# Performance work log

Measured on AMD Instinct MI355X. Metric: run time of the kernel, lower is better.

## Reference

```python
import jax, jax.numpy as jnp
import numpy as np

C = 64
CR = C // 8  # reduced channels for Q/K


def _conv1x1(x, W, b):
    # 1x1 conv == per-pixel linear over channels: x [b,c,h,w], W [o,c], b [o]
    return jnp.einsum('bchw,oc->bohw', x, W) + b[None, :, None, None]


def setup_inputs() -> dict:
    key = jax.random.key(0)
    ks = jax.random.split(key, 12)
    b, c, h, w = 8, C, 48, 48
    s = 1.0 / np.sqrt(c)
    inp = {
        'x1': jax.random.normal(ks[0], (b, c, h, w), jnp.float32),
        'x2': jax.random.normal(ks[1], (b, c, h, w), jnp.float32),
        'Wqk1': jax.random.normal(ks[2], (2 * CR, c), jnp.float32) * s,
        'bqk1': jnp.zeros((2 * CR,), jnp.float32),
        'Wqk2': jax.random.normal(ks[3], (2 * CR, c), jnp.float32) * s,
        'bqk2': jnp.zeros((2 * CR,), jnp.float32),
        'Wv1': jax.random.normal(ks[4], (c, c), jnp.float32) * s,
        'bv1': jnp.zeros((c,), jnp.float32),
        'Wv2': jax.random.normal(ks[5], (c, c), jnp.float32) * s,
        'bv2': jnp.zeros((c,), jnp.float32),
        'gamma': jnp.zeros((1,), jnp.float32) + 0.1,  # nonzero so output depends on attn
        'beta': jnp.zeros((1,), jnp.float32) + 0.1,
    }
    return inp


def reference(x1, x2, Wqk1, bqk1, Wqk2, bqk2, Wv1, bv1, Wv2, bv2, gamma, beta):
    b, c, h, w = x1.shape
    n = h * w
    qk1 = _conv1x1(x1, Wqk1, bqk1)
    qk2 = _conv1x1(x2, Wqk2, bqk2)
    q1, k1 = qk1[:, :CR], qk1[:, CR:]
    q2, k2 = qk2[:, :CR], qk2[:, CR:]
    # flatten spatial: [b, cr, n]
    q1 = q1.reshape(b, CR, n); k1 = k1.reshape(b, CR, n)
    q2 = q2.reshape(b, CR, n); k2 = k2.reshape(b, CR, n)
    v1 = _conv1x1(x1, Wv1, bv1).reshape(b, c, n)
    v2 = _conv1x1(x2, Wv2, bv2).reshape(b, c, n)
    # attn[b,i,j] = softmax_j( q[:, :, i] . k[:, :, j] )
    attn1 = jax.nn.softmax(jnp.einsum('bci,bcj->bij', q1, k1), axis=-1)
    attn2 = jax.nn.softmax(jnp.einsum('bci,bcj->bij', q2, k2), axis=-1)
    # out[:, :, j] = sum_i v[:, :, i] * attn[:, i, j]
    o1 = jnp.einsum('bci,bij->bcj', v1, attn2).reshape(b, c, h, w) * gamma + x1
    o2 = jnp.einsum('bci,bij->bcj', v2, attn1).reshape(b, c, h, w) * beta + x2
    return (o1, o2)
```

## Files before the change

kernel.cpp:

```cpp
#include <hip/hip_runtime.h>
#include <hip/hip_bf16.h>

#define NB   8
#define CCH  64
#define CR8  8
#define NPX  2304
#define BCN  (NB*CCH*NPX)
#define LOG2E 1.4426950408889634f

typedef short  short8   __attribute__((ext_vector_type(8)));
typedef unsigned short ushort8t __attribute__((ext_vector_type(8)));
typedef float  float4t  __attribute__((ext_vector_type(4)));
typedef float  float16t __attribute__((ext_vector_type(16)));

static __device__ __forceinline__ float fexp2(float x) {
    return __builtin_amdgcn_exp2f(x);
}
static __device__ __forceinline__ unsigned short bf16r(float f) {
    return (unsigned short)((__float_as_uint(f) + 0x8000u) >> 16);
}
static __device__ __forceinline__ unsigned int pack_bf16(float lo, float hi) {
    const unsigned int ul = __float_as_uint(lo) + 0x8000u;
    const unsigned int uh = __float_as_uint(hi) + 0x8000u;
    return __builtin_amdgcn_perm(uh, ul, 0x07060302u);
}
static __device__ __forceinline__ short8 pack8(const float* f) {
    union { unsigned int u[4]; short8 s; } r;
    #pragma unroll
    for (int j = 0; j < 4; j++) r.u[j] = pack_bf16(f[2*j], f[2*j+1]);
    return r.s;
}

static __device__ __forceinline__ void build_bfrag(const float16t sc, short8* bf) {
    unsigned int d[4][2];
    #pragma unroll
    for (int q = 0; q < 4; q++) {
        #pragma unroll
        for (int m = 0; m < 2; m++)
            d[q][m] = pack_bf16(fexp2(sc[4*q + 2*m]), fexp2(sc[4*q + 2*m + 1]));
    }
    #pragma unroll
    for (int kp = 0; kp < 2; kp++) {
        union { unsigned int u[4]; short8 s; } r;
        #pragma unroll
        for (int m = 0; m < 2; m++) {
            unsigned int x = d[2*kp][m];
            unsigned int y = d[2*kp + 1][m];
            asm("v_permlane32_swap_b32 %0, %1" : "+v"(x), "+v"(y));
            r.u[m]     = x;
            r.u[2 + m] = y;
        }
        bf[kp] = r.s;
    }
}

#define WS_QB1 0
#define WS_KB1 (WS_QB1 + 147456)
#define WS_QB2 (WS_KB1 + 147456)
#define WS_KB2 (WS_QB2 + 147456)
#define WS_V1  (WS_KB2 + 147456)
#define WS_V2  (WS_V1 + BCN/2)
#define WS_PD  (WS_V2 + BCN/2)

__global__ __launch_bounds__(256) void proj_kernel(
    const float* __restrict__ x1, const float* __restrict__ x2,
    const float* __restrict__ Wqk1, const float* __restrict__ bqk1,
    const float* __restrict__ Wqk2, const float* __restrict__ bqk2,
    const float* __restrict__ Wv1,  const float* __restrict__ bv1,
    const float* __restrict__ Wv2,  const float* __restrict__ bv2,
    float* __restrict__ ws, float* __restrict__ out)
{
    const int t    = threadIdx.x;
    const int lane = t & 63;
    const int w    = t >> 6;
    const int n16  = lane & 15;
    const int c4   = lane >> 4;
    const int nt   = w & 1;
    const int mh   = w >> 1;
    const int b    = blockIdx.y;
    const int px   = blockIdx.x * 32 + nt * 16 + n16;

    const float* xsb[2];
    xsb[0] = x1 + ((size_t)b * CCH) * NPX + px;
    xsb[1] = x2 + ((size_t)b * CCH) * NPX + px;

    float xr[2][16];
    short8 bfrag[2][2];
    #pragma unroll
    for (int st = 0; st < 2; st++) {
        #pragma unroll
        for (int ch = 0; ch < 2; ch++) {
            #pragma unroll
            for (int j = 0; j < 8; j++)
                xr[st][ch * 8 + j] = xsb[st][(ch * 32 + c4 * 8 + j) * NPX];
            bfrag[st][ch] = pack8(&xr[st][ch * 8]);
        }
    }

    if (mh == 0) {
        #pragma unroll
        for (int st = 0; st < 2; st++) {
            float* outs = out + (st ? (size_t)BCN : 0);
            #pragma unroll
            for (int e = 0; e < 16; e++) {
                const int ch = (e >> 3) * 32 + c4 * 8 + (e & 7);
                outs[((size_t)b * CCH + ch) * NPX + px] = xr[st][e];
            }
        }
    }

    float4t acc[5];
    #pragma unroll
    for (int mt = 0; mt < 5; mt++) { acc[mt][0]=0.f; acc[mt][1]=0.f; acc[mt][2]=0.f; acc[mt][3]=0.f; }

    #pragma unroll
    for (int mt = 0; mt < 5; mt++) {
        const int mi  = mh * 5 + mt;
        const int isqk = (mi < 2);
        const int st  = isqk ? (mi & 1) : (mi >= 6);
        const float* Wb;
        int rowbase;
        if (isqk) { Wb = (mi == 0) ? Wqk1 : Wqk2; rowbase = 0; }
        else      { Wb = (mi >= 6) ? Wv2 : Wv1; rowbase = (mi - (mi >= 6 ? 6 : 2)) * 16; }
        const float* wrow = Wb + (size_t)(rowbase + n16) * 64 + c4 * 8;

        const short8 bf0 = st ? bfrag[1][0] : bfrag[0][0];
        const short8 bf1 = st ? bfrag[1][1] : bfrag[0][1];

        #pragma unroll
        for (int ch = 0; ch < 2; ch++) {
            float fa[8];
            const float4 a0 = *(const float4*)(wrow + ch * 32);
            const float4 a1 = *(const float4*)(wrow + ch * 32 + 4);
            fa[0] = a0.x; fa[1] = a0.y; fa[2] = a0.z; fa[3] = a0.w;
            fa[4] = a1.x; fa[5] = a1.y; fa[6] = a1.z; fa[7] = a1.w;
            acc[mt] = __builtin_amdgcn_mfma_f32_16x16x32_bf16(
                pack8(fa), ch ? bf1 : bf0, acc[mt], 0, 0, 0);
        }
    }

    #pragma unroll
    for (int mt = 0; mt < 5; mt++) {
        const int mi = mh * 5 + mt;
        if (mi < 2) {
            const int st = mi & 1;
            const float* bqk = st ? bqk2 : bqk1;
            unsigned short* qb = (unsigned short*)(ws + (st ? WS_QB2 : WS_QB1));
            unsigned short* kb = (unsigned short*)(ws + (st ? WS_KB2 : WS_KB1));
            const size_t rbase = (size_t)(b * NPX + px) * 16;
            #pragma unroll
            for (int r = 0; r < 4; r++) {
                const int oc = c4 * 4 + r;
                const float val = acc[mt][r] + bqk[oc];
                if (oc < 8)
                    qb[rbase + oc] = bf16r(val * LOG2E);
                else
                    kb[rbase + (oc - 8)] = bf16r(val);
            }
            ushort8t zq, zk;
            #pragma unroll
            for (int e = 0; e < 8; e++) { zq[e] = 0; zk[e] = 0; }
            zk[0] = 0x3F80; zk[1] = 0x3F80;
            if (c4 == 0) *(ushort8t*)(qb + rbase + 8) = zq;
            if (c4 == 2) *(ushort8t*)(kb + rbase + 8) = zk;
        } else {
            const int st = (mi >= 6);
            const int vt_ = mi - (st ? 6 : 2);
            const float* bv = st ? bv2 : bv1;
            unsigned short* v = (unsigned short*)(ws + (st ? WS_V2 : WS_V1));
            #pragma unroll
            for (int r = 0; r < 4; r++) {
                const int oc = vt_ * 16 + c4 * 4 + r;
                const float val = acc[mt][r] + bv[oc];
                v[((size_t)b * CCH + oc) * NPX + px] = bf16r(val);
            }
        }
    }
}

__global__ __launch_bounds__(256) void stats_kernel(float* __restrict__ ws)
{
    const int t  = threadIdx.x;
    const int w  = t >> 6;
    const int n  = t & 31;
    const int h  = (t & 63) >> 5;
    const int jsb = blockIdx.x;
    const int iq  = blockIdx.y;
    const int ab  = blockIdx.z;
    const int b   = ab & 7;
    const int a   = ab >> 3;

    const unsigned short* qb = (const unsigned short*)(ws + (a ? WS_QB2 : WS_QB1));
    const unsigned short* kb = (const unsigned short*)(ws + (a ? WS_KB2 : WS_KB1));
    float* pd = ws + WS_PD;

    __shared__ float red[4][288];

    const int j = jsb * 128 + w * 32 + n;
    const short8 kfrag = *(const short8*)(kb + (size_t)(b * NPX + j) * 16 + h * 8);

    const unsigned short* qp = qb + (size_t)(b * NPX + iq * 288 + n) * 16 + h * 8;
    short8 qf = *(const short8*)qp;

    for (int ib = 0; ib < 9; ib++) {
        qp += 512;
        short8 qn = qf;
        if (ib + 1 < 9) qn = *(const short8*)qp;
        float16t acc = {};
        acc = __builtin_amdgcn_mfma_f32_32x32x16_bf16(kfrag, qf, acc, 0, 0, 0);
        float s0 = 0.f, s1 = 0.f, s2 = 0.f, s3 = 0.f;
        #pragma unroll
        for (int r = 0; r < 4; r++) {
            s0 += fexp2(acc[4 * r + 0]);
            s1 += fexp2(acc[4 * r + 1]);
            s2 += fexp2(acc[4 * r + 2]);
            s3 += fexp2(acc[4 * r + 3]);
        }
        float ssum = (s0 + s1) + (s2 + s3);
        ssum += __shfl_xor(ssum, 32);
        if (h == 0) red[w][ib * 32 + n] = ssum;
        qf = qn;
    }
    __syncthreads();
    for (int idx = t; idx < 288; idx += 256)
        pd[((size_t)ab * 18 + jsb) * NPX + iq * 288 + idx] =
            red[0][idx] + red[1][idx] + red[2][idx] + red[3][idx];
}

__global__ __launch_bounds__(256) void merge_fold(float* __restrict__ ws)
{
    const float* pd = ws + WS_PD;
    const int t  = threadIdx.x;
    const int il = t & 63;
    const int pg = t >> 6;
    const int i  = blockIdx.x * 64 + il;
    const int ab = blockIdx.y;
    const int b  = ab & 7;
    const int a  = ab >> 3;

    __shared__ float red[4][64];

    const float* pb = pd + (size_t)ab * 18 * NPX + i;
    float d = 0.f;
    #pragma unroll
    for (int c = pg; c < 18; c += 4)
        d += pb[(size_t)c * NPX];
    red[pg][il] = d;
    __syncthreads();

    if (t < 64) {
        const float dt = (red[0][t] + red[1][t]) + (red[2][t] + red[3][t]);
        const float m = -__log2f(dt);
        const unsigned short mh = bf16r(m);
        __hip_bfloat16 hb; *(unsigned short*)&hb = mh;
        const unsigned short ml = bf16r(m - __bfloat162float(hb));
        unsigned short* qb = (unsigned short*)(ws + (a ? WS_QB2 : WS_QB1));
        const size_t rbase = (size_t)(b * NPX + blockIdx.x * 64 + t) * 16;
        qb[rbase + 8] = mh;
        qb[rbase + 9] = ml;
    }
}

__global__ __launch_bounds__(256) void out_kernel(
    const float* __restrict__ gamma, const float* __restrict__ beta,
    const float* __restrict__ ws, float* __restrict__ out)
{
    const int t  = threadIdx.x;
    const int jt = blockIdx.x;
    const int b  = blockIdx.y;
    const int z  = blockIdx.z;
    const int o  = z >> 2;
    const int ihalf = z & 3;

    const int a = o ? 0 : 1;
    const unsigned short* qb = (const unsigned short*)(ws + (a ? WS_QB2 : WS_QB1));
    const unsigned short* kb = (const unsigned short*)(ws + (a ? WS_KB2 : WS_KB1));
    const unsigned short* v  = (const unsigned short*)(ws + (o ? WS_V2 : WS_V1));
    const float  scale = o ? beta[0] : gamma[0];

    __shared__ unsigned short vt[2][64][72];

    const int lane = t & 63;
    const int w    = t >> 6;
    const int n    = lane & 31;
    const int h    = lane >> 5;
    const int jh   = w & 1;
    const int ih   = w >> 1;

    const int j0 = jt * 64 + jh * 32;

    const short8 kfrag = *(const short8*)(kb + (size_t)(b * NPX + j0 + n) * 16 + h * 8);

    const int c0 = t >> 3, s80 = (t & 7) * 8;
    const int c1 = (t + 256) >> 3, s81 = ((t + 256) & 7) * 8;

    const int ibase = ihalf * 576;
    const unsigned short* vp0 = v + ((size_t)b * CCH + c0) * NPX + ibase + s80;
    const unsigned short* vp1 = v + ((size_t)b * CCH + c1) * NPX + ibase + s81;
    const unsigned short* qp  = qb + (size_t)(b * NPX + ibase + ih * 32 + n) * 16 + h * 8;

    {
        const float4 va = *(const float4*)vp0;
        const float4 vb = *(const float4*)vp1;
        *(float4*)&vt[0][c0][s80] = va;
        *(float4*)&vt[0][c1][s81] = vb;
    }
    short8 qf = *(const short8*)qp;

    float16t oacc0 = {}, oacc1 = {};
    int cur = 0;

    for (int it = 0; it < 9; it++) {
        vp0 += 64; vp1 += 64; qp += 64 * 16;
        float4 vn0, vn1;
        short8 qn = qf;
        if (it + 1 < 9) {
            vn0 = *(const float4*)vp0;
            vn1 = *(const float4*)vp1;
            qn  = *(const short8*)qp;
        }

        __syncthreads();

        float16t sc = {};
        sc = __builtin_amdgcn_mfma_f32_32x32x16_bf16(qf, kfrag, sc, 0, 0, 0);

        short8 bf[2];
        build_bfrag(sc, bf);

        {
            const short8 a0 = *(const short8*)&vt[cur][n][ih * 32 + 0 * 16 + h * 8];
            const short8 a1 = *(const short8*)&vt[cur][32 + n][ih * 32 + 0 * 16 + h * 8];
            oacc0 = __builtin_amdgcn_mfma_f32_32x32x16_bf16(a0, bf[0], oacc0, 0, 0, 0);
            oacc1 = __builtin_amdgcn_mfma_f32_32x32x16_bf16(a1, bf[0], oacc1, 0, 0, 0);
            const short8 a2 = *(const short8*)&vt[cur][n][ih * 32 + 1 * 16 + h * 8];
            const short8 a3 = *(const short8*)&vt[cur][32 + n][ih * 32 + 1 * 16 + h * 8];
            oacc0 = __builtin_amdgcn_mfma_f32_32x32x16_bf16(a2, bf[1], oacc0, 0, 0, 0);
            oacc1 = __builtin_amdgcn_mfma_f32_32x32x16_bf16(a3, bf[1], oacc1, 0, 0, 0);
        }

        if (it + 1 < 9) {
            *(float4*)&vt[cur ^ 1][c0][s80] = vn0;
            *(float4*)&vt[cur ^ 1][c1][s81] = vn1;
        }

        qf = qn;
        cur ^= 1;
    }

    __syncthreads();
    float* comb = (float*)&vt[0][0][0];
    float* cb = comb + (size_t)jh * 2304 + (size_t)lane * 36;
    if (ih == 1) {
        *(float4*)(cb +  0) = *((const float4*)&oacc0 + 0);
        *(float4*)(cb +  4) = *((const float4*)&oacc0 + 1);
        *(float4*)(cb +  8) = *((const float4*)&oacc0 + 2);
        *(float4*)(cb + 12) = *((const float4*)&oacc0 + 3);
        *(float4*)(cb + 16) = *((const float4*)&oacc1 + 0);
        *(float4*)(cb + 20) = *((const float4*)&oacc1 + 1);
        *(float4*)(cb + 24) = *((const float4*)&oacc1 + 2);
        *(float4*)(cb + 28) = *((const float4*)&oacc1 + 3);
    }
    __syncthreads();
    if (ih == 0) {
        #pragma unroll
        for (int q = 0; q < 4; q++) {
            const float4 p0 = *(const float4*)(cb + q * 4);
            const float4 p1 = *(const float4*)(cb + 16 + q * 4);
            oacc0[4*q+0] += p0.x; oacc0[4*q+1] += p0.y; oacc0[4*q+2] += p0.z; oacc0[4*q+3] += p0.w;
            oacc1[4*q+0] += p1.x; oacc1[4*q+1] += p1.y; oacc1[4*q+2] += p1.z; oacc1[4*q+3] += p1.w;
        }
        float* outp = out + (o ? BCN : 0) + (b * CCH) * NPX + j0 + n;
        #pragma unroll
        for (int r = 0; r < 16; r++) {
            const int row = (r & 3) + 8 * (r >> 2) + 4 * h;
            atomicAdd(outp + row * NPX, oacc0[r] * scale);
            atomicAdd(outp + (32 + row) * NPX, oacc1[r] * scale);
        }
    }
}

extern "C" void kernel_launch(void* const* d_in, const int* in_sizes, int n_in,
                              void* d_out, int out_size, void* d_ws, size_t ws_size,
                              hipStream_t stream)
{
    const float* x1   = (const float*)d_in[0];
    const float* x2   = (const float*)d_in[1];
    const float* Wqk1 = (const float*)d_in[2];
    const float* bqk1 = (const float*)d_in[3];
    const float* Wqk2 = (const float*)d_in[4];
    const float* bqk2 = (const float*)d_in[5];
    const float* Wv1  = (const float*)d_in[6];
    const float* bv1  = (const float*)d_in[7];
    const float* Wv2  = (const float*)d_in[8];
    const float* bv2  = (const float*)d_in[9];
    const float* gamma = (const float*)d_in[10];
    const float* beta  = (const float*)d_in[11];
    float* out = (float*)d_out;
    float* ws  = (float*)d_ws;

    proj_kernel<<<dim3(72, 8), 256, 0, stream>>>(
        x1, x2, Wqk1, bqk1, Wqk2, bqk2, Wv1, bv1, Wv2, bv2, ws, out);
    stats_kernel<<<dim3(18, 8, 16), 256, 0, stream>>>(ws);
    merge_fold<<<dim3(36, 16), 256, 0, stream>>>(ws);
    out_kernel<<<dim3(36, 8, 8), 256, 0, stream>>>(gamma, beta, ws, out);
}
```

Measured before the change: 148.1 us.

## Fuse stats, merge and output kernels into persistent kernel with grid barriers

Replaces three separate launches (row-sum stats, merge/fold of softmax denominators, output attention-V product) with one persistent kernel of 1024 blocks that loops over work items and separates phases with atomic-counter global barriers. Barrier counters are reset by the projection kernel. The aim is to remove launch gaps and kernel-boundary drains between short phases. In exchange it needs all 1024 blocks co-resident (launch bounds 256,4 with 256 CUs) or the barrier deadlocks, and each barrier adds spin-wait cost.

```diff
diff --git a/kernel.cpp b/kernel.cpp
--- a/kernel.cpp
+++ b/kernel.cpp
@@ -61,6 +61,21 @@
 #define WS_V1  (WS_KB2 + 147456)
 #define WS_V2  (WS_V1 + BCN/2)
 #define WS_PD  (WS_V2 + BCN/2)
+#define WS_BAR (WS_PD + 16*18*NPX)
+
+#define FUSED_GRID 1024
+
+static __device__ __forceinline__ void gbar(unsigned int* bar, unsigned int target) {
+    __syncthreads();
+    if (threadIdx.x == 0) {
+        __threadfence();
+        __hip_atomic_fetch_add(bar, 1u, __ATOMIC_RELEASE, __HIP_MEMORY_SCOPE_AGENT);
+        while (__hip_atomic_load(bar, __ATOMIC_ACQUIRE, __HIP_MEMORY_SCOPE_AGENT) < target)
+            __builtin_amdgcn_s_sleep(2);
+        __threadfence();
+    }
+    __syncthreads();
+}
 
 __global__ __launch_bounds__(256) void proj_kernel(
     const float* __restrict__ x1, const float* __restrict__ x2,
@@ -80,6 +95,11 @@
     const int b    = blockIdx.y;
     const int px   = blockIdx.x * 32 + nt * 16 + n16;
 
+    if (blockIdx.x == 0 && blockIdx.y == 0 && t == 0) {
+        unsigned int* bar = (unsigned int*)(ws + WS_BAR);
+        bar[0] = 0; bar[1] = 0;
+    }
+
     const float* xsb[2];
     xsb[0] = x1 + ((size_t)b * CCH) * NPX + px;
     xsb[1] = x2 + ((size_t)b * CCH) * NPX + px;
@@ -178,204 +198,223 @@
     }
 }
 
-__global__ __launch_bounds__(256) void stats_kernel(float* __restrict__ ws)
+__global__ __launch_bounds__(256, 4) void fused_smo(
+    const float* __restrict__ gamma, const float* __restrict__ beta,
+    float* __restrict__ ws, float* __restrict__ out)
 {
-    const int t  = threadIdx.x;
-    const int w  = t >> 6;
-    const int n  = t & 31;
-    const int h  = (t & 63) >> 5;
-    const int jsb = blockIdx.x;
-    const int iq  = blockIdx.y;
-    const int ab  = blockIdx.z;
-    const int b   = ab & 7;
-    const int a   = ab >> 3;
-
-    const unsigned short* qb = (const unsigned short*)(ws + (a ? WS_QB2 : WS_QB1));
-    const unsigned short* kb = (const unsigned short*)(ws + (a ? WS_KB2 : WS_KB1));
-    float* pd = ws + WS_PD;
-
-    __shared__ float red[4][288];
-
-    const int j = jsb * 128 + w * 32 + n;
-    const short8 kfrag = *(const short8*)(kb + (size_t)(b * NPX + j) * 16 + h * 8);
-
-    const unsigned short* qp = qb + (size_t)(b * NPX + iq * 288 + n) * 16 + h * 8;
-    short8 qf = *(const short8*)qp;
-
-    for (int ib = 0; ib < 9; ib++) {
-        qp += 512;
-        short8 qn = qf;
-        if (ib + 1 < 9) qn = *(const short8*)qp;
-        float16t acc = {};
-        acc = __builtin_amdgcn_mfma_f32_32x32x16_bf16(kfrag, qf, acc, 0, 0, 0);
-        float s0 = 0.f, s1 = 0.f, s2 = 0.f, s3 = 0.f;
-        #pragma unroll
-        for (int r = 0; r < 4; r++) {
-            s0 += fexp2(acc[4 * r + 0]);
-            s1 += fexp2(acc[4 * r + 1]);
-            s2 += fexp2(acc[4 * r + 2]);
-            s3 += fexp2(acc[4 * r + 3]);
-        }
-        float ssum = (s0 + s1) + (s2 + s3);
-        ssum += __shfl_xor(ssum, 32);
-        if (h == 0) red[w][ib * 32 + n] = ssum;
-        qf = qn;
-    }
-    __syncthreads();
-    for (int idx = t; idx < 288; idx += 256)
-        pd[((size_t)ab * 18 + jsb) * NPX + iq * 288 + idx] =
-            red[0][idx] + red[1][idx] + red[2][idx] + red[3][idx];
-}
-
-__global__ __launch_bounds__(256) void merge_fold(float* __restrict__ ws)
-{
-    const float* pd = ws + WS_PD;
-    const int t  = threadIdx.x;
-    const int il = t & 63;
-    const int pg = t >> 6;
-    const int i  = blockIdx.x * 64 + il;
-    const int ab = blockIdx.y;
-    const int b  = ab & 7;
-    const int a  = ab >> 3;
-
-    __shared__ float red[4][64];
-
-    const float* pb = pd + (size_t)ab * 18 * NPX + i;
-    float d = 0.f;
-    #pragma unroll
-    for (int c = pg; c < 18; c += 4)
-        d += pb[(size_t)c * NPX];
-    red[pg][il] = d;
-    __syncthreads();
-
-    if (t < 64) {
-        const float dt = (red[0][t] + red[1][t]) + (red[2][t] + red[3][t]);
-        const float m = -__log2f(dt);
-        const unsigned short mh = bf16r(m);
-        __hip_bfloat16 hb; *(unsigned short*)&hb = mh;
-        const unsigned short ml = bf16r(m - __bfloat162float(hb));
-        unsigned short* qb = (unsigned short*)(ws + (a ? WS_QB2 : WS_QB1));
-        const size_t rbase = (size_t)(b * NPX + blockIdx.x * 64 + t) * 16;
-        qb[rbase + 8] = mh;
-        qb[rbase + 9] = ml;
-    }
-}
-
-__global__ __launch_bounds__(256) void out_kernel(
-    const float* __restrict__ gamma, const float* __restrict__ beta,
-    const float* __restrict__ ws, float* __restrict__ out)
-{
-    const int t  = threadIdx.x;
-    const int jt = blockIdx.x;
-    const int b  = blockIdx.y;
-    const int z  = blockIdx.z;
-    const int o  = z >> 2;
-    const int ihalf = z & 3;
-
-    const int a = o ? 0 : 1;
-    const unsigned short* qb = (const unsigned short*)(ws + (a ? WS_QB2 : WS_QB1));
-    const unsigned short* kb = (const unsigned short*)(ws + (a ? WS_KB2 : WS_KB1));
-    const unsigned short* v  = (const unsigned short*)(ws + (o ? WS_V2 : WS_V1));
-    const float  scale = o ? beta[0] : gamma[0];
-
-    __shared__ unsigned short vt[2][64][72];
-
-    const int lane = t & 63;
-    const int w    = t >> 6;
-    const int n    = lane & 31;
-    const int h    = lane >> 5;
-    const int jh   = w & 1;
-    const int ih   = w >> 1;
-
-    const int j0 = jt * 64 + jh * 32;
-
-    const short8 kfrag = *(const short8*)(kb + (size_t)(b * NPX + j0 + n) * 16 + h * 8);
-
-    const int c0 = t >> 3, s80 = (t & 7) * 8;
-    const int c1 = (t + 256) >> 3, s81 = ((t + 256) & 7) * 8;
-
-    const int ibase = ihalf * 576;
-    const unsigned short* vp0 = v + ((size_t)b * CCH + c0) * NPX + ibase + s80;
-    const unsigned short* vp1 = v + ((size_t)b * CCH + c1) * NPX + ibase + s81;
-    const unsigned short* qp  = qb + (size_t)(b * NPX + ibase + ih * 32 + n) * 16 + h * 8;
+    __shared__ __align__(16) char sh[18432];
+    const int t   = threadIdx.x;
+    const int bid = blockIdx.x;
+    unsigned int* bar = (unsigned int*)(ws + WS_BAR);
 
     {
-        const float4 va = *(const float4*)vp0;
-        const float4 vb = *(const float4*)vp1;
-        *(float4*)&vt[0][c0][s80] = va;
-        *(float4*)&vt[0][c1][s81] = vb;
-    }
-    short8 qf = *(const short8*)qp;
-
-    float16t oacc0 = {}, oacc1 = {};
-    int cur = 0;
-
-    for (int it = 0; it < 9; it++) {
-        vp0 += 64; vp1 += 64; qp += 64 * 16;
-        float4 vn0, vn1;
-        short8 qn = qf;
-        if (it + 1 < 9) {
-            vn0 = *(const float4*)vp0;
-            vn1 = *(const float4*)vp1;
-            qn  = *(const short8*)qp;
-        }
-
-        __syncthreads();
-
-        float16t sc = {};
-        sc = __builtin_amdgcn_mfma_f32_32x32x16_bf16(qf, kfrag, sc, 0, 0, 0);
-
-        short8 bf[2];
-        build_bfrag(sc, bf);
-
-        {
-            const short8 a0 = *(const short8*)&vt[cur][n][ih * 32 + 0 * 16 + h * 8];
-            const short8 a1 = *(const short8*)&vt[cur][32 + n][ih * 32 + 0 * 16 + h * 8];
-            oacc0 = __builtin_amdgcn_mfma_f32_32x32x16_bf16(a0, bf[0], oacc0, 0, 0, 0);
-            oacc1 = __builtin_amdgcn_mfma_f32_32x32x16_bf16(a1, bf[0], oacc1, 0, 0, 0);
-            const short8 a2 = *(const short8*)&vt[cur][n][ih * 32 + 1 * 16 + h * 8];
-            const short8 a3 = *(const short8*)&vt[cur][32 + n][ih * 32 + 1 * 16 + h * 8];
-            oacc0 = __builtin_amdgcn_mfma_f32_32x32x16_bf16(a2, bf[1], oacc0, 0, 0, 0);
-            oacc1 = __builtin_amdgcn_mfma_f32_32x32x16_bf16(a3, bf[1], oacc1, 0, 0, 0);
-        }
-
-        if (it + 1 < 9) {
-            *(float4*)&vt[cur ^ 1][c0][s80] = vn0;
-            *(float4*)&vt[cur ^ 1][c1][s81] = vn1;
-        }
-
-        qf = qn;
-        cur ^= 1;
-    }
-
-    __syncthreads();
-    float* comb = (float*)&vt[0][0][0];
-    float* cb = comb + (size_t)jh * 2304 + (size_t)lane * 36;
-    if (ih == 1) {
-        *(float4*)(cb +  0) = *((const float4*)&oacc0 + 0);
-        *(float4*)(cb +  4) = *((const float4*)&oacc0 + 1);
-        *(float4*)(cb +  8) = *((const float4*)&oacc0 + 2);
-        *(float4*)(cb + 12) = *((const float4*)&oacc0 + 3);
-        *(float4*)(cb + 16) = *((const float4*)&oacc1 + 0);
-        *(float4*)(cb + 20) = *((const float4*)&oacc1 + 1);
-        *(float4*)(cb + 24) = *((const float4*)&oacc1 + 2);
-        *(float4*)(cb + 28) = *((const float4*)&oacc1 + 3);
-    }
-    __syncthreads();
-    if (ih == 0) {
-        #pragma unroll
-        for (int q = 0; q < 4; q++) {
-            const float4 p0 = *(const float4*)(cb + q * 4);
-            const float4 p1 = *(const float4*)(cb + 16 + q * 4);
-            oacc0[4*q+0] += p0.x; oacc0[4*q+1] += p0.y; oacc0[4*q+2] += p0.z; oacc0[4*q+3] += p0.w;
-            oacc1[4*q+0] += p1.x; oacc1[4*q+1] += p1.y; oacc1[4*q+2] += p1.z; oacc1[4*q+3] += p1.w;
-        }
-        float* outp = out + (o ? BCN : 0) + (b * CCH) * NPX + j0 + n;
-        #pragma unroll
-        for (int r = 0; r < 16; r++) {
-            const int row = (r & 3) + 8 * (r >> 2) + 4 * h;
-            atomicAdd(outp + row * NPX, oacc0[r] * scale);
-            atomicAdd(outp + (32 + row) * NPX, oacc1[r] * scale);
+        float (*red)[288] = (float (*)[288])sh;
+        const int w  = t >> 6;
+        const int n  = t & 31;
+        const int h  = (t & 63) >> 5;
+        float* pd = ws + WS_PD;
+
+        for (int item = bid; item < 18 * 8 * 16; item += FUSED_GRID) {
+            const int jsb = item % 18;
+            const int rest = item / 18;
+            const int iq  = rest & 7;
+            const int ab  = rest >> 3;
+            const int b   = ab & 7;
+            const int a   = ab >> 3;
+
+            __syncthreads();
+
+            const unsigned short* qb = (const unsigned short*)(ws + (a ? WS_QB2 : WS_QB1));
+            const unsigned short* kb = (const unsigned short*)(ws + (a ? WS_KB2 : WS_KB1));
+
+            const int j = jsb * 128 + w * 32 + n;
+            const short8 kfrag = *(const short8*)(kb + (size_t)(b * NPX + j) * 16 + h * 8);
+
+            const unsigned short* qp = qb + (size_t)(b * NPX + iq * 288 + n) * 16 + h * 8;
+            short8 qf = *(const short8*)qp;
+
+            for (int ib = 0; ib < 9; ib++) {
+                qp += 512;
+                short8 qn = qf;
+                if (ib + 1 < 9) qn = *(const short8*)qp;
+                float16t acc = {};
+                acc = __builtin_amdgcn_mfma_f32_32x32x16_bf16(kfrag, qf, acc, 0, 0, 0);
+                float s0 = 0.f, s1 = 0.f, s2 = 0.f, s3 = 0.f;
+                #pragma unroll
+                for (int r = 0; r < 4; r++) {
+                    s0 += fexp2(acc[4 * r + 0]);
+                    s1 += fexp2(acc[4 * r + 1]);
+                    s2 += fexp2(acc[4 * r + 2]);
+                    s3 += fexp2(acc[4 * r + 3]);
+                }
+                float ssum = (s0 + s1) + (s2 + s3);
+                ssum += __shfl_xor(ssum, 32);
+                if (h == 0) red[w][ib * 32 + n] = ssum;
+                qf = qn;
+            }
+            __syncthreads();
+            for (int idx = t; idx < 288; idx += 256)
+                pd[((size_t)ab * 18 + jsb) * NPX + iq * 288 + idx] =
+                    red[0][idx] + red[1][idx] + red[2][idx] + red[3][idx];
+        }
+    }
+
+    gbar(&bar[0], (unsigned int)gridDim.x);
+
+    {
+        float (*red)[64] = (float (*)[64])sh;
+        const float* pd = ws + WS_PD;
+        const int il = t & 63;
+        const int pg = t >> 6;
+
+        for (int item = bid; item < 36 * 16; item += FUSED_GRID) {
+            const int igrp = item % 36;
+            const int ab   = item / 36;
+            const int b    = ab & 7;
+            const int a    = ab >> 3;
+            const int i    = igrp * 64 + il;
+
+            __syncthreads();
+
+            const float* pb = pd + (size_t)ab * 18 * NPX + i;
+            float d = 0.f;
+            #pragma unroll
+            for (int c = pg; c < 18; c += 4)
+                d += pb[(size_t)c * NPX];
+            red[pg][il] = d;
+            __syncthreads();
+
+            if (t < 64) {
+                const float dt = (red[0][t] + red[1][t]) + (red[2][t] + red[3][t]);
+                const float m = -__log2f(dt);
+                const unsigned short mh = bf16r(m);
+                __hip_bfloat16 hb; *(unsigned short*)&hb = mh;
+                const unsigned short ml = bf16r(m - __bfloat162float(hb));
+                unsigned short* qb = (unsigned short*)(ws + (a ? WS_QB2 : WS_QB1));
+                const size_t rbase = (size_t)(b * NPX + igrp * 64 + t) * 16;
+                qb[rbase + 8] = mh;
+                qb[rbase + 9] = ml;
+            }
+        }
+    }
+
+    gbar(&bar[1], (unsigned int)gridDim.x);
+
+    {
+        unsigned short (*vt)[64][72] = (unsigned short (*)[64][72])sh;
+        const int lane = t & 63;
+        const int w    = t >> 6;
+        const int n    = lane & 31;
+        const int h    = lane >> 5;
+        const int jh   = w & 1;
+        const int ih   = w >> 1;
+        const int c0 = t >> 3, s80 = (t & 7) * 8;
+        const int c1 = (t + 256) >> 3, s81 = ((t + 256) & 7) * 8;
+
+        for (int item = bid; item < 36 * 8 * 8; item += FUSED_GRID) {
+            const int jt = item % 36;
+            const int rest = item / 36;
+            const int b  = rest & 7;
+            const int z  = rest >> 3;
+            const int o  = z >> 2;
+            const int ihalf = z & 3;
+
+            __syncthreads();
+
+            const int a = o ? 0 : 1;
+            const unsigned short* qb = (const unsigned short*)(ws + (a ? WS_QB2 : WS_QB1));
+            const unsigned short* kb = (const unsigned short*)(ws + (a ? WS_KB2 : WS_KB1));
+            const unsigned short* v  = (const unsigned short*)(ws + (o ? WS_V2 : WS_V1));
+            const float scale = o ? beta[0] : gamma[0];
+
+            const int j0 = jt * 64 + jh * 32;
+
+            const short8 kfrag = *(const short8*)(kb + (size_t)(b * NPX + j0 + n) * 16 + h * 8);
+
+            const int ibase = ihalf * 576;
+            const unsigned short* vp0 = v + ((size_t)b * CCH + c0) * NPX + ibase + s80;
+            const unsigned short* vp1 = v + ((size_t)b * CCH + c1) * NPX + ibase + s81;
+            const unsigned short* qp  = qb + (size_t)(b * NPX + ibase + ih * 32 + n) * 16 + h * 8;
+
+            {
+                const float4 va = *(const float4*)vp0;
+                const float4 vb = *(const float4*)vp1;
+                *(float4*)&vt[0][c0][s80] = va;
+                *(float4*)&vt[0][c1][s81] = vb;
+            }
+            short8 qf = *(const short8*)qp;
+
+            float16t oacc0 = {}, oacc1 = {};
+            int cur = 0;
+
+            for (int it = 0; it < 9; it++) {
+                vp0 += 64; vp1 += 64; qp += 64 * 16;
+                float4 vn0, vn1;
+                short8 qn = qf;
+                if (it + 1 < 9) {
+                    vn0 = *(const float4*)vp0;
+                    vn1 = *(const float4*)vp1;
+                    qn  = *(const short8*)qp;
+                }
+
+                __syncthreads();
+
+                float16t sc = {};
+                sc = __builtin_amdgcn_mfma_f32_32x32x16_bf16(qf, kfrag, sc, 0, 0, 0);
+
+                short8 bf[2];
+                build_bfrag(sc, bf);
+
+                {
+                    const short8 a0 = *(const short8*)&vt[cur][n][ih * 32 + 0 * 16 + h * 8];
+                    const short8 a1 = *(const short8*)&vt[cur][32 + n][ih * 32 + 0 * 16 + h * 8];
+                    oacc0 = __builtin_amdgcn_mfma_f32_32x32x16_bf16(a0, bf[0], oacc0, 0, 0, 0);
+                    oacc1 = __builtin_amdgcn_mfma_f32_32x32x16_bf16(a1, bf[0], oacc1, 0, 0, 0);
+                    const short8 a2 = *(const short8*)&vt[cur][n][ih * 32 + 1 * 16 + h * 8];
+                    const short8 a3 = *(const short8*)&vt[cur][32 + n][ih * 32 + 1 * 16 + h * 8];
+                    oacc0 = __builtin_amdgcn_mfma_f32_32x32x16_bf16(a2, bf[1], oacc0, 0, 0, 0);
+                    oacc1 = __builtin_amdgcn_mfma_f32_32x32x16_bf16(a3, bf[1], oacc1, 0, 0, 0);
+                }
+
+                if (it + 1 < 9) {
+                    *(float4*)&vt[cur ^ 1][c0][s80] = vn0;
+                    *(float4*)&vt[cur ^ 1][c1][s81] = vn1;
+                }
+
+                qf = qn;
+                cur ^= 1;
+            }
+
+            __syncthreads();
+            float* comb = (float*)sh;
+            float* cb = comb + (size_t)jh * 2304 + (size_t)lane * 36;
+            if (ih == 1) {
+                *(float4*)(cb +  0) = *((const float4*)&oacc0 + 0);
+                *(float4*)(cb +  4) = *((const float4*)&oacc0 + 1);
+                *(float4*)(cb +  8) = *((const float4*)&oacc0 + 2);
+                *(float4*)(cb + 12) = *((const float4*)&oacc0 + 3);
+                *(float4*)(cb + 16) = *((const float4*)&oacc1 + 0);
+                *(float4*)(cb + 20) = *((const float4*)&oacc1 + 1);
+                *(float4*)(cb + 24) = *((const float4*)&oacc1 + 2);
+                *(float4*)(cb + 28) = *((const float4*)&oacc1 + 3);
+            }
+            __syncthreads();
+            if (ih == 0) {
+                #pragma unroll
+                for (int q = 0; q < 4; q++) {
+                    const float4 p0 = *(const float4*)(cb + q * 4);
+                    const float4 p1 = *(const float4*)(cb + 16 + q * 4);
+                    oacc0[4*q+0] += p0.x; oacc0[4*q+1] += p0.y; oacc0[4*q+2] += p0.z; oacc0[4*q+3] += p0.w;
+                    oacc1[4*q+0] += p1.x; oacc1[4*q+1] += p1.y; oacc1[4*q+2] += p1.z; oacc1[4*q+3] += p1.w;
+                }
+                float* outp = out + (o ? BCN : 0) + (b * CCH) * NPX + j0 + n;
+                #pragma unroll
+                for (int r = 0; r < 16; r++) {
+                    const int row = (r & 3) + 8 * (r >> 2) + 4 * h;
+                    atomicAdd(outp + row * NPX, oacc0[r] * scale);
+                    atomicAdd(outp + (32 + row) * NPX, oacc1[r] * scale);
+                }
+            }
         }
     }
 }
@@ -401,7 +440,5 @@
 
     proj_kernel<<<dim3(72, 8), 256, 0, stream>>>(
         x1, x2, Wqk1, bqk1, Wqk2, bqk2, Wv1, bv1, Wv2, bv2, ws, out);
-    stats_kernel<<<dim3(18, 8, 16), 256, 0, stream>>>(ws);
-    merge_fold<<<dim3(36, 16), 256, 0, stream>>>(ws);
-    out_kernel<<<dim3(36, 8, 8), 256, 0, stream>>>(gamma, beta, ws, out);
-}
+    fused_smo<<<dim3(FUSED_GRID), 256, 0, stream>>>(gamma, beta, ws, out);
+}
```

New measurement: 430.6 us. 2.91x slower.

## Fuse softmax-denominator merge into stats kernel via last-block atomic counter

Applied to the files above, without the earlier changes.

Removes the separate merge_fold launch. Each stats block bumps an atomic counter for its (ab, iq) group, and the last of the 18 blocks sums the partial denominators and writes the log-normalizer into the Q buffer. This saves one kernel launch and its dependency gap. In exchange it adds threadfences, an atomic, and a serial tail of work in the last block per group. The counters are zeroed inside proj_kernel.

```diff
diff --git a/kernel.cpp b/kernel.cpp
--- a/kernel.cpp
+++ b/kernel.cpp
@@ -61,6 +61,7 @@
 #define WS_V1  (WS_KB2 + 147456)
 #define WS_V2  (WS_V1 + BCN/2)
 #define WS_PD  (WS_V2 + BCN/2)
+#define WS_CNT (WS_PD + 16*18*NPX)
 
 __global__ __launch_bounds__(256) void proj_kernel(
     const float* __restrict__ x1, const float* __restrict__ x2,
@@ -80,6 +81,9 @@
     const int b    = blockIdx.y;
     const int px   = blockIdx.x * 32 + nt * 16 + n16;
 
+    if (blockIdx.x == 0 && blockIdx.y == 0 && t < 128)
+        ((unsigned int*)(ws + WS_CNT))[t] = 0;
+
     const float* xsb[2];
     xsb[0] = x1 + ((size_t)b * CCH) * NPX + px;
     xsb[1] = x2 + ((size_t)b * CCH) * NPX + px;
@@ -195,6 +199,7 @@
     float* pd = ws + WS_PD;
 
     __shared__ float red[4][288];
+    __shared__ int is_last;
 
     const int j = jsb * 128 + w * 32 + n;
     const short8 kfrag = *(const short8*)(kb + (size_t)(b * NPX + j) * 16 + h * 8);
@@ -225,39 +230,34 @@
     for (int idx = t; idx < 288; idx += 256)
         pd[((size_t)ab * 18 + jsb) * NPX + iq * 288 + idx] =
             red[0][idx] + red[1][idx] + red[2][idx] + red[3][idx];
-}
-
-__global__ __launch_bounds__(256) void merge_fold(float* __restrict__ ws)
-{
-    const float* pd = ws + WS_PD;
-    const int t  = threadIdx.x;
-    const int il = t & 63;
-    const int pg = t >> 6;
-    const int i  = blockIdx.x * 64 + il;
-    const int ab = blockIdx.y;
-    const int b  = ab & 7;
-    const int a  = ab >> 3;
-
-    __shared__ float red[4][64];
-
-    const float* pb = pd + (size_t)ab * 18 * NPX + i;
-    float d = 0.f;
-    #pragma unroll
-    for (int c = pg; c < 18; c += 4)
-        d += pb[(size_t)c * NPX];
-    red[pg][il] = d;
+
     __syncthreads();
-
-    if (t < 64) {
-        const float dt = (red[0][t] + red[1][t]) + (red[2][t] + red[3][t]);
-        const float m = -__log2f(dt);
-        const unsigned short mh = bf16r(m);
-        __hip_bfloat16 hb; *(unsigned short*)&hb = mh;
-        const unsigned short ml = bf16r(m - __bfloat162float(hb));
-        unsigned short* qb = (unsigned short*)(ws + (a ? WS_QB2 : WS_QB1));
-        const size_t rbase = (size_t)(b * NPX + blockIdx.x * 64 + t) * 16;
-        qb[rbase + 8] = mh;
-        qb[rbase + 9] = ml;
+    if (t == 0) {
+        __threadfence();
+        unsigned int* cnt = (unsigned int*)(ws + WS_CNT);
+        const unsigned int prev = __hip_atomic_fetch_add(
+            &cnt[ab * 8 + iq], 1u, __ATOMIC_ACQ_REL, __HIP_MEMORY_SCOPE_AGENT);
+        is_last = (prev == 17);
+    }
+    __syncthreads();
+    if (is_last) {
+        __threadfence();
+        unsigned short* qbw = (unsigned short*)(ws + (a ? WS_QB2 : WS_QB1));
+        for (int idx = t; idx < 288; idx += 256) {
+            const int i = iq * 288 + idx;
+            const float* pb = pd + (size_t)ab * 18 * NPX + i;
+            float d = 0.f;
+            #pragma unroll
+            for (int c = 0; c < 18; c++)
+                d += pb[(size_t)c * NPX];
+            const float m = -__log2f(d);
+            const unsigned short mhi = bf16r(m);
+            __hip_bfloat16 hb; *(unsigned short*)&hb = mhi;
+            const unsigned short mlo = bf16r(m - __bfloat162float(hb));
+            const size_t rbase = (size_t)(b * NPX + i) * 16;
+            qbw[rbase + 8] = mhi;
+            qbw[rbase + 9] = mlo;
+        }
     }
 }
 
@@ -402,6 +402,5 @@
     proj_kernel<<<dim3(72, 8), 256, 0, stream>>>(
         x1, x2, Wqk1, bqk1, Wqk2, bqk2, Wv1, bv1, Wv2, bv2, ws, out);
     stats_kernel<<<dim3(18, 8, 16), 256, 0, stream>>>(ws);
-    merge_fold<<<dim3(36, 16), 256, 0, stream>>>(ws);
     out_kernel<<<dim3(36, 8, 8), 256, 0, stream>>>(gamma, beta, ws, out);
 }
```

Result: slower. 289.4 us (+95.4%).
